# Optimization experiments

Hardware: AMD Instinct MI355X
Metric: run time of the kernel (lower is better)

The kernel has to match this reference:

```python
import jax, jax.numpy as jnp
import numpy as np

B, L, C = 4, 2048, 1024

def setup_inputs() -> dict:
    key = jax.random.key(0)
    k1, k2, k3 = jax.random.split(key, 3)
    net_in = jax.random.normal(k1, (B, L, C), dtype=jnp.float32)
    # torch Linear weights stored as (out, in); we keep that convention
    w_qkv = jax.random.normal(k2, (3 * C, C), dtype=jnp.float32) * (1.0 / np.sqrt(C))
    w_out = jax.random.normal(k3, (C, C), dtype=jnp.float32) * (1.0 / np.sqrt(C))
    return {"net_in": net_in, "w_qkv": w_qkv, "w_out": w_out}

def reference(net_in, w_qkv, w_out):
    Bc, Lc, Cc = net_in.shape
    qkv = jnp.einsum('blc,dc->bld', net_in, w_qkv)  # (B, L, 3C)
    q, k, v = jnp.split(qkv, 3, axis=-1)
    attn = jnp.einsum('bqc,bkc->bqk', q, k) / jnp.sqrt(jnp.float32(Cc))
    causal = jnp.tril(jnp.ones((Lc, Lc), dtype=bool))
    attn = jnp.where(causal[None, :, :], attn, -jnp.inf)
    attn = jax.nn.softmax(attn, axis=-1)
    out = jnp.einsum('bqk,bkc->bqc', attn, v)
    return jnp.einsum('blc,dc->bld', out, w_out)
```

## Files before the change

kernel.cpp:

```cpp
#include <hip/hip_runtime.h>
#include <hip/hip_bf16.h>
#include <cstdint>
#include <cstddef>

typedef __hip_bfloat16 bf16;
typedef float  floatx4 __attribute__((ext_vector_type(4)));
typedef __bf16 bf16x8  __attribute__((ext_vector_type(8)));

typedef __attribute__((address_space(1))) void as1_void;
typedef __attribute__((address_space(3))) void as3_void;

constexpr int Bn = 4, Ln = 2048, Cn = 1024;

__device__ __forceinline__ void store_one(float* p, float v) { *p = v; }
__device__ __forceinline__ void store_one(bf16*  p, float v) { *p = __float2bfloat16(v); }

template <typename OutT>
__device__ __forceinline__ void gemm_core(
    const bf16* __restrict__ A, const bf16* __restrict__ B, OutT* __restrict__ C,
    int m0, int n0, int Keff, int lda, int ldb, int ldc, float cscale)
{
    __shared__ __align__(16) bf16 smem[2 * 128 * 32];

    const int tid  = threadIdx.x;
    const int lane = tid & 63;
    const int quad = lane >> 4;
    const int lr   = lane & 15;
    const int wave = tid >> 6;
    const int wm   = (wave >> 1) * 64;
    const int wn   = (wave & 1) * 64;

    floatx4 acc[4][4];
#pragma unroll
    for (int i = 0; i < 4; ++i)
#pragma unroll
        for (int j = 0; j < 4; ++j) { floatx4 z = {0.f, 0.f, 0.f, 0.f}; acc[i][j] = z; }

    const bf16* gbase[4];
    int ldsoff[4];
#pragma unroll
    for (int it = 0; it < 4; ++it) {
        int chunk = it * 256 + tid;
        ldsoff[it] = __builtin_amdgcn_readfirstlane((chunk & ~63) * 16);
        int kc = chunk & 3;
        if (chunk < 512) {
            int m = chunk >> 2;
            gbase[it] = A + (size_t)(m0 + m) * lda + kc * 8;
        } else {
            int c2 = chunk - 512;
            int n = c2 >> 2;
            gbase[it] = B + (size_t)(n0 + n) * ldb + kc * 8;
        }
    }

    for (int k0 = 0; k0 < Keff; k0 += 32) {
        __syncthreads();
#pragma unroll
        for (int it = 0; it < 4; ++it) {
            uintptr_t ga = (uintptr_t)(gbase[it] + k0);
            uintptr_t la = (uintptr_t)((char*)smem + ldsoff[it]);
            __builtin_amdgcn_global_load_lds((const as1_void*)ga, (as3_void*)la, 16, 0, 0);
        }
        __syncthreads();

        const bf16* As = smem;
        const bf16* Bs = smem + 128 * 32;
        bf16x8 afrag[4], bfrag[4];
#pragma unroll
        for (int i = 0; i < 4; ++i)
            afrag[i] = *(const bf16x8*)(As + (size_t)(wm + i * 16 + lr) * 32 + quad * 8);
#pragma unroll
        for (int j = 0; j < 4; ++j)
            bfrag[j] = *(const bf16x8*)(Bs + (size_t)(wn + j * 16 + lr) * 32 + quad * 8);
#pragma unroll
        for (int i = 0; i < 4; ++i)
#pragma unroll
            for (int j = 0; j < 4; ++j)
                acc[i][j] = __builtin_amdgcn_mfma_f32_16x16x32_bf16(afrag[i], bfrag[j], acc[i][j], 0, 0, 0);
    }

#pragma unroll
    for (int i = 0; i < 4; ++i) {
        int row = m0 + wm + i * 16 + quad * 4;
#pragma unroll
        for (int j = 0; j < 4; ++j) {
            int col = n0 + wn + j * 16 + lr;
            OutT* cp = C + (size_t)row * ldc + col;
#pragma unroll
            for (int r = 0; r < 4; ++r)
                store_one(cp + (size_t)r * ldc, acc[i][j][r] * cscale);
        }
    }
}

__global__ __launch_bounds__(256)
void g1_w2_qk(const bf16* __restrict__ Xb, const bf16* __restrict__ Wqkb,
              const bf16* __restrict__ Wob, const bf16* __restrict__ WvT,
              bf16* __restrict__ QK, bf16* __restrict__ W2)
{
    int i = blockIdx.x;
    if (i < 64) {
        int m0 = (i & 7) * 128, n0 = (i >> 3) * 128;
        gemm_core<bf16>(Wob, WvT, W2, m0, n0, 1024, 1024, 1024, 1024, 1.0f);
    } else {
        int j = i - 64;
        int m0 = (j & 63) * 128, n0 = (j >> 6) * 128;
        gemm_core<bf16>(Xb, Wqkb, QK, m0, n0, 1024, 1024, 1024, 2048, 1.0f);
    }
}

__global__ __launch_bounds__(256)
void g2_vwt_s(const bf16* __restrict__ W2, const bf16* __restrict__ Xb,
              const bf16* __restrict__ QK, bf16* __restrict__ VWT,
              bf16* __restrict__ S)
{
    int i = blockIdx.x;
    if (i < 512) {
        int m0 = (i & 7) * 128, n0 = (i >> 3) * 128;
        gemm_core<bf16>(W2, Xb, VWT, m0, n0, 1024, 1024, 1024, 8192, 1.0f);
    } else {
        int j = i - 512;
        int b = j / 136, t = j - b * 136;
        int ti = (int)((sqrtf(8.f * t + 1.f) - 1.f) * 0.5f);
        while ((ti + 1) * (ti + 2) / 2 <= t) ++ti;
        while (ti * (ti + 1) / 2 > t) --ti;
        int tj = t - ti * (ti + 1) / 2;
        const bf16* Aq = QK + (long long)b * Ln * 2048;
        const bf16* Bk = Aq + 1024;
        bf16* Sb = S + (long long)b * Ln * Ln;
        gemm_core<bf16>(Aq, Bk, Sb, ti * 128, tj * 128, 1024, 2048, 2048, Ln, 0.03125f);
    }
}

__global__ __launch_bounds__(256)
void g3_out(const bf16* __restrict__ P, const bf16* __restrict__ VWT,
            float* __restrict__ out)
{
    int i = blockIdx.x;
    int b = i >> 7, r = i & 127;
    int mt = 15 - (r >> 3), nt = r & 7;
    int m0 = mt * 128, n0 = nt * 128;
    const bf16* Pp = P + (long long)b * Ln * Ln;
    const bf16* Bv = VWT + b * Ln;
    float* Co = out + (long long)b * Ln * Cn;
    gemm_core<float>(Pp, Bv, Co, m0, n0, m0 + 128, Ln, 8192, Cn, 1.0f);
}

__device__ __forceinline__ float waveMax(float x) {
#pragma unroll
    for (int o = 32; o > 0; o >>= 1) x = fmaxf(x, __shfl_xor(x, o, 64));
    return x;
}
__device__ __forceinline__ float waveSum(float x) {
#pragma unroll
    for (int o = 32; o > 0; o >>= 1) x += __shfl_xor(x, o, 64);
    return x;
}

__global__ __launch_bounds__(256)
void softmax_causal(bf16* __restrict__ S)
{
    const int wave = threadIdx.x >> 6, lane = threadIdx.x & 63;
    const int row = blockIdx.x * 4 + wave;
    const int q = row & (Ln - 1);
    bf16* Srow = S + (long long)row * Ln;
    const int kmax = ((q >> 7) + 1) << 7;
    const int nv = (kmax + 511) >> 9;

    float x[4][8];
    float m = -1e30f;
    for (int it = 0; it < nv; ++it) {
        int c0 = it * 512 + lane * 8;
        bf16x8 v = *(const bf16x8*)(Srow + c0);
#pragma unroll
        for (int e = 0; e < 8; ++e) {
            float f = (float)v[e];
            f = (c0 + e <= q) ? f : -1e30f;
            x[it][e] = f;
            m = fmaxf(m, f);
        }
    }
    m = waveMax(m);
    float s = 0.f;
    for (int it = 0; it < nv; ++it)
#pragma unroll
        for (int e = 0; e < 8; ++e) {
            float ex = (x[it][e] > -1e29f) ? __expf(x[it][e] - m) : 0.f;
            x[it][e] = ex;
            s += ex;
        }
    s = waveSum(s);
    float inv = 1.f / s;
    for (int it = 0; it < nv; ++it) {
        bf16x8 o;
#pragma unroll
        for (int e = 0; e < 8; ++e) o[e] = (__bf16)(x[it][e] * inv);
        *(bf16x8*)(Srow + it * 512 + lane * 8) = o;
    }
}

__global__ __launch_bounds__(256)
void cast_all(const float* __restrict__ X, const float* __restrict__ Wqkv,
              const float* __restrict__ Wo,
              bf16* __restrict__ Xb, bf16* __restrict__ Wqkb,
              bf16* __restrict__ Wob, bf16* __restrict__ WvT)
{
    int blk = blockIdx.x;
    if (blk < 11264) {
        int i = blk * 256 + threadIdx.x;
        const float* src; bf16* dst; int off;
        if (i < 2097152)                 { src = X;    dst = Xb;   off = i; }
        else if (i < 2097152 + 524288)   { src = Wqkv; dst = Wqkb; off = i - 2097152; }
        else                             { src = Wo;   dst = Wob;  off = i - 2621440; }
        float4 f = ((const float4*)src)[off];
        bf16 o0 = __float2bfloat16(f.x), o1 = __float2bfloat16(f.y);
        bf16 o2 = __float2bfloat16(f.z), o3 = __float2bfloat16(f.w);
        ushort4 u;
        u.x = *(unsigned short*)&o0; u.y = *(unsigned short*)&o1;
        u.z = *(unsigned short*)&o2; u.w = *(unsigned short*)&o3;
        *(ushort4*)(dst + (size_t)off * 4) = u;
    } else {
        __shared__ float t[32][33];
        int tt = blk - 11264;
        int c0 = (tt & 31) * 32;
        int r0 = (tt >> 5) * 32;
        const float* Wv = Wqkv + 2048 * 1024;
        int xcol = threadIdx.x & 31, y0 = threadIdx.x >> 5;
#pragma unroll
        for (int p = 0; p < 4; ++p) {
            int y = y0 + 8 * p;
            t[y][xcol] = Wv[(size_t)(r0 + y) * 1024 + c0 + xcol];
        }
        __syncthreads();
#pragma unroll
        for (int p = 0; p < 4; ++p) {
            int mloc = y0 + 8 * p;
            WvT[(size_t)(c0 + mloc) * 1024 + r0 + xcol] = __float2bfloat16(t[xcol][mloc]);
        }
    }
}

extern "C" void kernel_launch(void* const* d_in, const int* in_sizes, int n_in,
                              void* d_out, int out_size, void* d_ws, size_t ws_size,
                              hipStream_t stream)
{
    const float* X    = (const float*)d_in[0];
    const float* Wqkv = (const float*)d_in[1];
    const float* Wout = (const float*)d_in[2];
    float* out = (float*)d_out;

    char* ws = (char*)d_ws;
    const size_t MiB = 1024ull * 1024ull;
    bf16* Xb   = (bf16*)(ws + 0);
    bf16* QK   = (bf16*)(ws + 16 * MiB);
    bf16* VWT  = (bf16*)(ws + 48 * MiB);
    bf16* Sbuf = (bf16*)(ws + 64 * MiB);
    bf16* Wqkb = (bf16*)(ws + 96 * MiB);
    bf16* WvT  = (bf16*)(ws + 100 * MiB);
    bf16* Wob  = (bf16*)(ws + 102 * MiB);
    bf16* W2   = (bf16*)(ws + 104 * MiB);

    cast_all<<<dim3(12288), 256, 0, stream>>>(X, Wqkv, Wout, Xb, Wqkb, Wob, WvT);

    g1_w2_qk<<<dim3(1088), 256, 0, stream>>>(Xb, Wqkb, Wob, WvT, QK, W2);

    g2_vwt_s<<<dim3(1056), 256, 0, stream>>>(W2, Xb, QK, VWT, Sbuf);

    softmax_causal<<<dim3(Bn * Ln / 4), 256, 0, stream>>>(Sbuf);

    g3_out<<<dim3(512), 256, 0, stream>>>(Sbuf, VWT, out);
}
```

Measured before the change: 271.9 us.

## Fuse all stages into one persistent kernel with software grid barriers

```diff
diff --git a/kernel.cpp b/kernel.cpp
--- a/kernel.cpp
+++ b/kernel.cpp
@@ -11,17 +11,30 @@
 typedef __attribute__((address_space(3))) void as3_void;
 
 constexpr int Bn = 4, Ln = 2048, Cn = 1024;
+constexpr int GRID = 512;
 
 __device__ __forceinline__ void store_one(float* p, float v) { *p = v; }
 __device__ __forceinline__ void store_one(bf16*  p, float v) { *p = __float2bfloat16(v); }
 
+__device__ __forceinline__ void gbar(int* cnt, int target)
+{
+    __syncthreads();
+    if (threadIdx.x == 0) {
+        __threadfence();
+        atomicAdd(cnt, 1);
+        while (atomicAdd(cnt, 0) < target)
+            __builtin_amdgcn_s_sleep(8);
+        __threadfence();
+    }
+    __syncthreads();
+}
+
 template <typename OutT>
 __device__ __forceinline__ void gemm_core(
+    bf16* smem,
     const bf16* __restrict__ A, const bf16* __restrict__ B, OutT* __restrict__ C,
     int m0, int n0, int Keff, int lda, int ldb, int ldc, float cscale)
 {
-    __shared__ __align__(16) bf16 smem[2 * 128 * 32];
-
     const int tid  = threadIdx.x;
     const int lane = tid & 63;
     const int quad = lane >> 4;
@@ -93,59 +106,6 @@
     }
 }
 
-__global__ __launch_bounds__(256)
-void g1_w2_qk(const bf16* __restrict__ Xb, const bf16* __restrict__ Wqkb,
-              const bf16* __restrict__ Wob, const bf16* __restrict__ WvT,
-              bf16* __restrict__ QK, bf16* __restrict__ W2)
-{
-    int i = blockIdx.x;
-    if (i < 64) {
-        int m0 = (i & 7) * 128, n0 = (i >> 3) * 128;
-        gemm_core<bf16>(Wob, WvT, W2, m0, n0, 1024, 1024, 1024, 1024, 1.0f);
-    } else {
-        int j = i - 64;
-        int m0 = (j & 63) * 128, n0 = (j >> 6) * 128;
-        gemm_core<bf16>(Xb, Wqkb, QK, m0, n0, 1024, 1024, 1024, 2048, 1.0f);
-    }
-}
-
-__global__ __launch_bounds__(256)
-void g2_vwt_s(const bf16* __restrict__ W2, const bf16* __restrict__ Xb,
-              const bf16* __restrict__ QK, bf16* __restrict__ VWT,
-              bf16* __restrict__ S)
-{
-    int i = blockIdx.x;
-    if (i < 512) {
-        int m0 = (i & 7) * 128, n0 = (i >> 3) * 128;
-        gemm_core<bf16>(W2, Xb, VWT, m0, n0, 1024, 1024, 1024, 8192, 1.0f);
-    } else {
-        int j = i - 512;
-        int b = j / 136, t = j - b * 136;
-        int ti = (int)((sqrtf(8.f * t + 1.f) - 1.f) * 0.5f);
-        while ((ti + 1) * (ti + 2) / 2 <= t) ++ti;
-        while (ti * (ti + 1) / 2 > t) --ti;
-        int tj = t - ti * (ti + 1) / 2;
-        const bf16* Aq = QK + (long long)b * Ln * 2048;
-        const bf16* Bk = Aq + 1024;
-        bf16* Sb = S + (long long)b * Ln * Ln;
-        gemm_core<bf16>(Aq, Bk, Sb, ti * 128, tj * 128, 1024, 2048, 2048, Ln, 0.03125f);
-    }
-}
-
-__global__ __launch_bounds__(256)
-void g3_out(const bf16* __restrict__ P, const bf16* __restrict__ VWT,
-            float* __restrict__ out)
-{
-    int i = blockIdx.x;
-    int b = i >> 7, r = i & 127;
-    int mt = 15 - (r >> 3), nt = r & 7;
-    int m0 = mt * 128, n0 = nt * 128;
-    const bf16* Pp = P + (long long)b * Ln * Ln;
-    const bf16* Bv = VWT + b * Ln;
-    float* Co = out + (long long)b * Ln * Cn;
-    gemm_core<float>(Pp, Bv, Co, m0, n0, m0 + 128, Ln, 8192, Cn, 1.0f);
-}
-
 __device__ __forceinline__ float waveMax(float x) {
 #pragma unroll
     for (int o = 32; o > 0; o >>= 1) x = fmaxf(x, __shfl_xor(x, o, 64));
@@ -157,86 +117,149 @@
     return x;
 }
 
-__global__ __launch_bounds__(256)
-void softmax_causal(bf16* __restrict__ S)
-{
-    const int wave = threadIdx.x >> 6, lane = threadIdx.x & 63;
-    const int row = blockIdx.x * 4 + wave;
-    const int q = row & (Ln - 1);
-    bf16* Srow = S + (long long)row * Ln;
-    const int kmax = ((q >> 7) + 1) << 7;
-    const int nv = (kmax + 511) >> 9;
-
-    float x[4][8];
-    float m = -1e30f;
-    for (int it = 0; it < nv; ++it) {
-        int c0 = it * 512 + lane * 8;
-        bf16x8 v = *(const bf16x8*)(Srow + c0);
-#pragma unroll
-        for (int e = 0; e < 8; ++e) {
-            float f = (float)v[e];
-            f = (c0 + e <= q) ? f : -1e30f;
-            x[it][e] = f;
-            m = fmaxf(m, f);
-        }
-    }
-    m = waveMax(m);
-    float s = 0.f;
-    for (int it = 0; it < nv; ++it)
-#pragma unroll
-        for (int e = 0; e < 8; ++e) {
-            float ex = (x[it][e] > -1e29f) ? __expf(x[it][e] - m) : 0.f;
-            x[it][e] = ex;
-            s += ex;
-        }
-    s = waveSum(s);
-    float inv = 1.f / s;
-    for (int it = 0; it < nv; ++it) {
-        bf16x8 o;
-#pragma unroll
-        for (int e = 0; e < 8; ++e) o[e] = (__bf16)(x[it][e] * inv);
-        *(bf16x8*)(Srow + it * 512 + lane * 8) = o;
-    }
-}
-
-__global__ __launch_bounds__(256)
-void cast_all(const float* __restrict__ X, const float* __restrict__ Wqkv,
-              const float* __restrict__ Wo,
-              bf16* __restrict__ Xb, bf16* __restrict__ Wqkb,
-              bf16* __restrict__ Wob, bf16* __restrict__ WvT)
-{
-    int blk = blockIdx.x;
-    if (blk < 11264) {
-        int i = blk * 256 + threadIdx.x;
+struct Params {
+    const float *X, *Wqkv, *Wo;
+    bf16 *Xb, *Wqkb, *WvT, *Wob, *W2, *QK, *VWT, *S;
+    float *out;
+    int *bar;
+};
+
+__global__ __launch_bounds__(256, 2) void mega(Params p)
+{
+    const int blk = blockIdx.x;
+    const int tid = threadIdx.x;
+    __shared__ __align__(16) bf16 smem[2 * 128 * 32];
+
+    for (int u = blk * 256 + tid; u < 524288 + 262144; u += GRID * 256) {
         const float* src; bf16* dst; int off;
-        if (i < 2097152)                 { src = X;    dst = Xb;   off = i; }
-        else if (i < 2097152 + 524288)   { src = Wqkv; dst = Wqkb; off = i - 2097152; }
-        else                             { src = Wo;   dst = Wob;  off = i - 2621440; }
+        if (u < 524288) { src = p.Wqkv; dst = p.Wqkb; off = u; }
+        else            { src = p.Wo;   dst = p.Wob;  off = u - 524288; }
         float4 f = ((const float4*)src)[off];
         bf16 o0 = __float2bfloat16(f.x), o1 = __float2bfloat16(f.y);
         bf16 o2 = __float2bfloat16(f.z), o3 = __float2bfloat16(f.w);
-        ushort4 u;
-        u.x = *(unsigned short*)&o0; u.y = *(unsigned short*)&o1;
-        u.z = *(unsigned short*)&o2; u.w = *(unsigned short*)&o3;
-        *(ushort4*)(dst + (size_t)off * 4) = u;
+        ushort4 uu;
+        uu.x = *(unsigned short*)&o0; uu.y = *(unsigned short*)&o1;
+        uu.z = *(unsigned short*)&o2; uu.w = *(unsigned short*)&o3;
+        *(ushort4*)(dst + (size_t)off * 4) = uu;
+    }
+    {
+        float* t = (float*)smem;
+        const float* Wv = p.Wqkv + (size_t)2048 * 1024;
+        int xcol = tid & 31, y0 = tid >> 5;
+        for (int tt = blk; tt < 1024; tt += GRID) {
+            int c0 = (tt & 31) * 32, r0 = (tt >> 5) * 32;
+            __syncthreads();
+#pragma unroll
+            for (int q = 0; q < 4; ++q) {
+                int y = y0 + 8 * q;
+                t[y * 33 + xcol] = Wv[(size_t)(r0 + y) * 1024 + c0 + xcol];
+            }
+            __syncthreads();
+#pragma unroll
+            for (int q = 0; q < 4; ++q) {
+                int mloc = y0 + 8 * q;
+                p.WvT[(size_t)(c0 + mloc) * 1024 + r0 + xcol] =
+                    __float2bfloat16(t[xcol * 33 + mloc]);
+            }
+        }
+    }
+    gbar(p.bar, 1 * GRID);
+
+    if (blk < 64) {
+        int m0 = (blk & 7) * 128, n0 = (blk >> 3) * 128;
+        gemm_core<bf16>(smem, p.Wob, p.WvT, p.W2, m0, n0, 1024, 1024, 1024, 1024, 1.0f);
     } else {
-        __shared__ float t[32][33];
-        int tt = blk - 11264;
-        int c0 = (tt & 31) * 32;
-        int r0 = (tt >> 5) * 32;
-        const float* Wv = Wqkv + 2048 * 1024;
-        int xcol = threadIdx.x & 31, y0 = threadIdx.x >> 5;
-#pragma unroll
-        for (int p = 0; p < 4; ++p) {
-            int y = y0 + 8 * p;
-            t[y][xcol] = Wv[(size_t)(r0 + y) * 1024 + c0 + xcol];
-        }
-        __syncthreads();
-#pragma unroll
-        for (int p = 0; p < 4; ++p) {
-            int mloc = y0 + 8 * p;
-            WvT[(size_t)(c0 + mloc) * 1024 + r0 + xcol] = __float2bfloat16(t[xcol][mloc]);
-        }
+        for (int u = (blk - 64) * 256 + tid; u < 2097152; u += 448 * 256) {
+            float4 f = ((const float4*)p.X)[u];
+            bf16 o0 = __float2bfloat16(f.x), o1 = __float2bfloat16(f.y);
+            bf16 o2 = __float2bfloat16(f.z), o3 = __float2bfloat16(f.w);
+            ushort4 uu;
+            uu.x = *(unsigned short*)&o0; uu.y = *(unsigned short*)&o1;
+            uu.z = *(unsigned short*)&o2; uu.w = *(unsigned short*)&o3;
+            *(ushort4*)(p.Xb + (size_t)u * 4) = uu;
+        }
+    }
+    gbar(p.bar, 2 * GRID);
+
+    for (int t = blk; t < 1536; t += GRID) {
+        if (t < 1024) {
+            int m0 = (t & 63) * 128, n0 = (t >> 6) * 128;
+            gemm_core<bf16>(smem, p.Xb, p.Wqkb, p.QK, m0, n0, 1024, 1024, 1024, 2048, 1.0f);
+        } else {
+            int v = t - 1024;
+            int m0 = (v >> 6) * 128, n0 = (v & 63) * 128;
+            gemm_core<bf16>(smem, p.W2, p.Xb, p.VWT, m0, n0, 1024, 1024, 1024, 8192, 1.0f);
+        }
+    }
+    gbar(p.bar, 3 * GRID);
+
+    for (int s = blk; s < 544; s += GRID) {
+        int b = (s & 7) >> 1;
+        int pp = s & 1;
+        int tt = (s >> 3) * 2 + pp;
+        int ti = (int)((sqrtf(8.f * tt + 1.f) - 1.f) * 0.5f);
+        while ((ti + 1) * (ti + 2) / 2 <= tt) ++ti;
+        while (ti * (ti + 1) / 2 > tt) --ti;
+        int tj = tt - ti * (ti + 1) / 2;
+        const bf16* Aq = p.QK + (long long)b * Ln * 2048;
+        const bf16* Bk = Aq + 1024;
+        bf16* Sb = p.S + (long long)b * Ln * Ln;
+        gemm_core<bf16>(smem, Aq, Bk, Sb, ti * 128, tj * 128, 1024, 2048, 2048, Ln, 0.03125f);
+    }
+    gbar(p.bar, 4 * GRID);
+
+    {
+        const int wave = tid >> 6, lane = tid & 63;
+        for (int g = blk; g < 2048; g += GRID) {
+            const int row = g * 4 + wave;
+            const int q = row & (Ln - 1);
+            bf16* Srow = p.S + (long long)row * Ln;
+            const int kmax = ((q >> 7) + 1) << 7;
+            const int nv = (kmax + 511) >> 9;
+
+            float x[4][8];
+            float m = -1e30f;
+            for (int it = 0; it < nv; ++it) {
+                int c0 = it * 512 + lane * 8;
+                bf16x8 v = *(const bf16x8*)(Srow + c0);
+#pragma unroll
+                for (int e = 0; e < 8; ++e) {
+                    float f = (float)v[e];
+                    f = (c0 + e <= q) ? f : -1e30f;
+                    x[it][e] = f;
+                    m = fmaxf(m, f);
+                }
+            }
+            m = waveMax(m);
+            float sum = 0.f;
+            for (int it = 0; it < nv; ++it)
+#pragma unroll
+                for (int e = 0; e < 8; ++e) {
+                    float ex = (x[it][e] > -1e29f) ? __expf(x[it][e] - m) : 0.f;
+                    x[it][e] = ex;
+                    sum += ex;
+                }
+            sum = waveSum(sum);
+            float inv = 1.f / sum;
+            for (int it = 0; it < nv; ++it) {
+                bf16x8 o;
+#pragma unroll
+                for (int e = 0; e < 8; ++e) o[e] = (__bf16)(x[it][e] * inv);
+                *(bf16x8*)(Srow + it * 512 + lane * 8) = o;
+            }
+        }
+    }
+    gbar(p.bar, 5 * GRID);
+
+    {
+        int r = blk & 7, q2 = blk >> 3;
+        int b = r >> 1, pp = r & 1;
+        int mt = 15 - (q2 >> 2), nt = pp + 2 * (q2 & 3);
+        int m0 = mt * 128, n0 = nt * 128;
+        const bf16* Pp = p.S + (long long)b * Ln * Ln;
+        const bf16* Bv = p.VWT + b * Ln;
+        float* Co = p.out + (long long)b * Ln * Cn;
+        gemm_core<float>(smem, Pp, Bv, Co, m0, n0, m0 + 128, Ln, 8192, Cn, 1.0f);
     }
 }
 
@@ -251,22 +274,18 @@
 
     char* ws = (char*)d_ws;
     const size_t MiB = 1024ull * 1024ull;
-    bf16* Xb   = (bf16*)(ws + 0);
-    bf16* QK   = (bf16*)(ws + 16 * MiB);
-    bf16* VWT  = (bf16*)(ws + 48 * MiB);
-    bf16* Sbuf = (bf16*)(ws + 64 * MiB);
-    bf16* Wqkb = (bf16*)(ws + 96 * MiB);
-    bf16* WvT  = (bf16*)(ws + 100 * MiB);
-    bf16* Wob  = (bf16*)(ws + 102 * MiB);
-    bf16* W2   = (bf16*)(ws + 104 * MiB);
-
-    cast_all<<<dim3(12288), 256, 0, stream>>>(X, Wqkv, Wout, Xb, Wqkb, Wob, WvT);
-
-    g1_w2_qk<<<dim3(1088), 256, 0, stream>>>(Xb, Wqkb, Wob, WvT, QK, W2);
-
-    g2_vwt_s<<<dim3(1056), 256, 0, stream>>>(W2, Xb, QK, VWT, Sbuf);
-
-    softmax_causal<<<dim3(Bn * Ln / 4), 256, 0, stream>>>(Sbuf);
-
-    g3_out<<<dim3(512), 256, 0, stream>>>(Sbuf, VWT, out);
-}
+    Params p;
+    p.X    = X;  p.Wqkv = Wqkv;  p.Wo = Wout;  p.out = out;
+    p.Xb   = (bf16*)(ws + 0);
+    p.QK   = (bf16*)(ws + 16 * MiB);
+    p.VWT  = (bf16*)(ws + 48 * MiB);
+    p.S    = (bf16*)(ws + 64 * MiB);
+    p.Wqkb = (bf16*)(ws + 96 * MiB);
+    p.WvT  = (bf16*)(ws + 100 * MiB);
+    p.Wob  = (bf16*)(ws + 102 * MiB);
+    p.W2   = (bf16*)(ws + 104 * MiB);
+    p.bar  = (int*)(ws + 106 * MiB);
+
+    hipMemsetAsync(p.bar, 0, 256, stream);
+    mega<<<dim3(GRID), dim3(256), 0, stream>>>(p);
+}
```

Result: slower. 566.9 us (+108.5%).
